# Kernel optimization log

Hardware: AMD Instinct MI355X
Metric: run time of the kernel (lower is better)

Reference implementation:

```python
import jax, jax.numpy as jnp
import numpy as np

N = 50000      # nodes
E = 800000     # edges (before self loops)
IN = 128       # input_dim
H1, C1 = 4, 64   # conv1 heads, per-head channels (concat -> 256)
H2, C2 = 1, 64   # conv2 heads, per-head channels (concat=False -> 64)
EPS_BN = 1e-5
NEG_SLOPE = 0.2


def setup_inputs() -> dict:
    key = jax.random.key(0)
    ks = jax.random.split(key, 20)
    s = 0.05
    d = {}
    d["x"] = jax.random.normal(ks[0], (N, IN), dtype=jnp.float32)
    d["edge_index"] = jax.random.randint(ks[1], (2, E), 0, N, dtype=jnp.int32)
    # GATConv 1: lin weight [IN, H1*C1], att vectors [H1, C1], bias [H1*C1]
    d["W1"] = jax.random.normal(ks[2], (IN, H1 * C1), dtype=jnp.float32) * s
    d["a1_src"] = jax.random.normal(ks[3], (H1, C1), dtype=jnp.float32) * s
    d["a1_dst"] = jax.random.normal(ks[4], (H1, C1), dtype=jnp.float32) * s
    d["b1"] = jnp.zeros((H1 * C1,), jnp.float32)
    # GATConv 2 (concat=False): lin weight [H1*C1, H2*C2]
    d["W2"] = jax.random.normal(ks[5], (H1 * C1, H2 * C2), dtype=jnp.float32) * s
    d["a2_src"] = jax.random.normal(ks[6], (H2, C2), dtype=jnp.float32) * s
    d["a2_dst"] = jax.random.normal(ks[7], (H2, C2), dtype=jnp.float32) * s
    d["b2"] = jnp.zeros((C2,), jnp.float32)
    # projection Linear(output_dim -> input_dim)
    d["Wp"] = jax.random.normal(ks[8], (C2, IN), dtype=jnp.float32) * s
    d["bp"] = jnp.zeros((IN,), jnp.float32)
    # BatchNorm affine params
    d["g1"] = jnp.ones((H1 * C1,), jnp.float32); d["be1"] = jnp.zeros((H1 * C1,), jnp.float32)
    d["g2"] = jnp.ones((C2,), jnp.float32);      d["be2"] = jnp.zeros((C2,), jnp.float32)
    d["g3"] = jnp.ones((IN,), jnp.float32);      d["be3"] = jnp.zeros((IN,), jnp.float32)
    return d


def batch_norm(x, gamma, beta):
    mu = jnp.mean(x, axis=0, keepdims=True)
    var = jnp.var(x, axis=0, keepdims=True)
    return (x - mu) * jax.lax.rsqrt(var + EPS_BN) * gamma + beta


def gat_conv(x, src, dst, W, a_src, a_dst, bias, heads, out_ch, concat):
    n = x.shape[0]
    h = (x @ W).reshape(n, heads, out_ch)            # [N,H,C]
    alpha_s = jnp.einsum('nhc,hc->nh', h, a_src)     # [N,H]
    alpha_d = jnp.einsum('nhc,hc->nh', h, a_dst)
    e = jax.nn.leaky_relu(alpha_s[src] + alpha_d[dst], NEG_SLOPE)  # [E',H]
    # segment softmax over edges sharing the same destination node
    m = jax.ops.segment_max(e, dst, num_segments=n)
    m = jnp.where(jnp.isfinite(m), m, 0.0)
    ex = jnp.exp(e - m[dst])
    den = jax.ops.segment_sum(ex, dst, num_segments=n)
    alpha = ex / (den[dst] + 1e-16)                  # [E',H]
    msg = alpha[:, :, None] * h[src]                 # [E',H,C]
    out = jax.ops.segment_sum(msg, dst, num_segments=n)  # [N,H,C]
    if concat:
        out = out.reshape(n, heads * out_ch)
    else:
        out = out.mean(axis=1)
    return out + bias


def reference(x, edge_index, W1, a1_src, a1_dst, b1, W2, a2_src, a2_dst, b2,
              Wp, bp, g1, be1, g2, be2, g3, be3):
    n = x.shape[0]
    # PyG GATConv default add_self_loops=True
    loops = jnp.arange(n, dtype=edge_index.dtype)
    src = jnp.concatenate([edge_index[0], loops])
    dst = jnp.concatenate([edge_index[1], loops])
    h = gat_conv(x, src, dst, W1, a1_src, a1_dst, b1, H1, C1, True)
    h = jax.nn.elu(batch_norm(h, g1, be1))
    # dropout is a no-op in eval mode
    h = gat_conv(h, src, dst, W2, a2_src, a2_dst, b2, H2, C2, False)
    h = jax.nn.elu(batch_norm(h, g2, be2))
    h = h @ Wp + bp
    return batch_norm(h, g3, be3)
```

## Files before the change

kernel.cpp:

```cpp
#include <hip/hip_runtime.h>
#include <cstdint>
#include <cstddef>

#define NEG_SLOPE 0.2f
#define EPS_BN 1e-5f

typedef __bf16 bf16x8 __attribute__((ext_vector_type(8)));
typedef float  f32x4  __attribute__((ext_vector_type(4)));
typedef unsigned short ushort_t;

static __device__ __forceinline__ float lrelu(float x){ return x > 0.f ? x : NEG_SLOPE * x; }
static __device__ __forceinline__ float elu(float x){ return x > 0.f ? x : __expf(x) - 1.f; }

static __device__ __forceinline__ float bf2f(ushort_t u){
  union { unsigned i; float f; } c; c.i = ((unsigned)u) << 16; return c.f;
}
static __device__ __forceinline__ ushort_t f2bf(float f){
  unsigned u = __float_as_uint(f);
  u += 0x7fffu + ((u >> 16) & 1u);
  return (ushort_t)(u >> 16);
}
static __device__ __forceinline__ void unpk(unsigned u, float& lo, float& hi){
  lo = __uint_as_float(u << 16);
  hi = __uint_as_float(u & 0xffff0000u);
}

union BF8 { bf16x8 v; ushort_t u[8]; };

static inline int ceil_div(int a, int b){ return (a + b - 1) / b; }


static __device__ void packW_body(const float* W, ushort_t* Wp, int K, int Nn, int idx){
  int lane = idx & 63;
  int rest = idx >> 6;
  int KS = K >> 5;
  int s = rest % KS, t = rest / KS;
  int n  = t * 16 + (lane & 15);
  int k0 = s * 32 + (lane >> 4) * 8;
  ushort_t tmp[8];
  #pragma unroll
  for(int j = 0; j < 8; j++) tmp[j] = f2bf(W[(size_t)(k0 + j) * Nn + n]);
  uint4 pk;
  pk.x = tmp[0] | ((unsigned)tmp[1] << 16);
  pk.y = tmp[2] | ((unsigned)tmp[3] << 16);
  pk.z = tmp[4] | ((unsigned)tmp[5] << 16);
  pk.w = tmp[6] | ((unsigned)tmp[7] << 16);
  *reinterpret_cast<uint4*>(Wp + (size_t)idx * 8) = pk;
}

__global__ void init_kernel(unsigned* __restrict__ zbase, int ztotal,
                            const float* __restrict__ W1, const float* __restrict__ W2,
                            const float* __restrict__ W3, ushort_t* __restrict__ W1p,
                            ushort_t* __restrict__ W2p, ushort_t* __restrict__ W3p){
  int b = blockIdx.x;
  if(b < 28){
    int idx = b * 256 + threadIdx.x;
    if(idx < 4096)       packW_body(W1, W1p, 128, 256, idx);
    else if(idx < 6144)  packW_body(W2, W2p, 256, 64,  idx - 4096);
    else if(idx < 7168)  packW_body(W3, W3p, 64,  128, idx - 6144);
  } else {
    int i = (b - 28) * 256 + threadIdx.x;
    if(i < ztotal) zbase[i] = 0u;
  }
}


template<int K, int NT, int AMODE, int H>
static __device__ __forceinline__ void gemm_body(int bx, const void* __restrict__ Asrc,
                                                 const ushort_t* __restrict__ Bp,
                                                 ushort_t* __restrict__ C, int M,
                                                 const float* __restrict__ scale,
                                                 const float* __restrict__ shift,
                                                 const float* __restrict__ a_src,
                                                 const float* __restrict__ a_dst,
                                                 float* __restrict__ as_,
                                                 float* __restrict__ ad_){
  constexpr int KS = K >> 5;
  int lane = threadIdx.x & 63, wv = threadIdx.x >> 6;
  int row0 = bx * 64 + wv * 16;
  int mi = lane & 15, q = lane >> 4;
  int arow = row0 + mi; if(arow > M - 1) arow = M - 1;
  const bf16x8* bbase = reinterpret_cast<const bf16x8*>(Bp) + lane;
  f32x4 acc[NT] = {};
  #pragma unroll
  for(int s = 0; s < KS; s++){
    BF8 cv;
    if(AMODE == 0){
      const float* ap = (const float*)Asrc + (size_t)arow * K + s * 32 + q * 8;
      float4 u0 = *reinterpret_cast<const float4*>(ap);
      float4 u1 = *reinterpret_cast<const float4*>(ap + 4);
      cv.u[0] = f2bf(u0.x); cv.u[1] = f2bf(u0.y); cv.u[2] = f2bf(u0.z); cv.u[3] = f2bf(u0.w);
      cv.u[4] = f2bf(u1.x); cv.u[5] = f2bf(u1.y); cv.u[6] = f2bf(u1.z); cv.u[7] = f2bf(u1.w);
    } else {
      const ushort_t* ap = (const ushort_t*)Asrc + (size_t)arow * K + s * 32 + q * 8;
      uint4 u = *reinterpret_cast<const uint4*>(ap);
      int c0 = s * 32 + q * 8;
      float4 sc0 = *reinterpret_cast<const float4*>(scale + c0);
      float4 sc1 = *reinterpret_cast<const float4*>(scale + c0 + 4);
      float4 sh0 = *reinterpret_cast<const float4*>(shift + c0);
      float4 sh1 = *reinterpret_cast<const float4*>(shift + c0 + 4);
      float a, b;
      unpk(u.x, a, b); cv.u[0] = f2bf(elu(a * sc0.x + sh0.x)); cv.u[1] = f2bf(elu(b * sc0.y + sh0.y));
      unpk(u.y, a, b); cv.u[2] = f2bf(elu(a * sc0.z + sh0.z)); cv.u[3] = f2bf(elu(b * sc0.w + sh0.w));
      unpk(u.z, a, b); cv.u[4] = f2bf(elu(a * sc1.x + sh1.x)); cv.u[5] = f2bf(elu(b * sc1.y + sh1.y));
      unpk(u.w, a, b); cv.u[6] = f2bf(elu(a * sc1.z + sh1.z)); cv.u[7] = f2bf(elu(b * sc1.w + sh1.w));
    }
    bf16x8 af = cv.v;
    #pragma unroll
    for(int t = 0; t < NT; t++){
      bf16x8 bfr = bbase[((size_t)t * KS + s) * 64];
      acc[t] = __builtin_amdgcn_mfma_f32_16x16x32_bf16(af, bfr, acc[t], 0, 0, 0);
    }
  }
  #pragma unroll
  for(int t = 0; t < NT; t++){
    #pragma unroll
    for(int r = 0; r < 4; r++){
      int gr = row0 + q * 4 + r;
      if(gr < M) C[(size_t)gr * (NT * 16) + t * 16 + mi] = f2bf(acc[t][r]);
    }
  }
  if(H > 0){
    #pragma unroll
    for(int hh = 0; hh < H; hh++){
      #pragma unroll
      for(int r = 0; r < 4; r++){
        float ps = 0.f, pd = 0.f;
        #pragma unroll
        for(int tt = 0; tt < 4; tt++){
          int t = hh * 4 + tt;
          float av = acc[t][r];
          int c = t * 16 + mi;
          ps += av * a_src[c];
          pd += av * a_dst[c];
        }
        #pragma unroll
        for(int off = 1; off < 16; off <<= 1){
          ps += __shfl_xor(ps, off);
          pd += __shfl_xor(pd, off);
        }
        int gr = row0 + q * 4 + r;
        if(mi == 0 && gr < M){
          as_[(size_t)gr * H + hh] = ps;
          ad_[(size_t)gr * H + hh] = pd;
        }
      }
    }
  }
}

template<int K, int NT, int AMODE, int H>
__global__ __launch_bounds__(256) void gemm_kernel(const void* __restrict__ Asrc,
                                                   const ushort_t* __restrict__ Bp,
                                                   ushort_t* __restrict__ C, int M,
                                                   const float* __restrict__ scale,
                                                   const float* __restrict__ shift,
                                                   const float* __restrict__ a_src,
                                                   const float* __restrict__ a_dst,
                                                   float* __restrict__ as_,
                                                   float* __restrict__ ad_){
  gemm_body<K, NT, AMODE, H>(blockIdx.x, Asrc, Bp, C, M, scale, shift, a_src, a_dst, as_, ad_);
}

__global__ __launch_bounds__(256) void hist_gemm1_kernel(int GB, const int* __restrict__ ei,
                                                         int* __restrict__ deg, int E, int N,
                                                         const float* __restrict__ x,
                                                         const ushort_t* __restrict__ W1p,
                                                         ushort_t* __restrict__ h1b,
                                                         const float* __restrict__ a1s,
                                                         const float* __restrict__ a1d,
                                                         float* __restrict__ as_,
                                                         float* __restrict__ ad_){
  int b = blockIdx.x;
  if(b < GB){
    gemm_body<128, 16, 0, 4>(b, x, W1p, h1b, N, nullptr, nullptr, a1s, a1d, as_, ad_);
  } else {
    int e = (b - GB) * 256 + threadIdx.x;
    if(e < E + N){
      int d = (e < E) ? ei[E + e] : (e - E);
      atomicAdd(&deg[d], 1);
    }
  }
}


__global__ __launch_bounds__(256) void scan1_kernel(const int* __restrict__ deg, int* __restrict__ rowptr,
                                                    int* __restrict__ partials,
                                                    unsigned* __restrict__ tick, int n){
  int t = threadIdx.x, lane = t & 63, wv = t >> 6;
  int base = blockIdx.x * 2048 + t * 8;
  int v[8]; int run = 0;
  #pragma unroll
  for(int k = 0; k < 8; k++){ int i = base + k; v[k] = (i < n) ? deg[i] : 0; run += v[k]; }
  int sc = run;
  #pragma unroll
  for(int off = 1; off < 64; off <<= 1){
    int u = __shfl_up(sc, off);
    if(lane >= off) sc += u;
  }
  __shared__ int wtot[4], woff[4];
  __shared__ bool slast;
  if(lane == 63) wtot[wv] = sc;
  __syncthreads();
  if(t == 0){
    int a = 0;
    #pragma unroll
    for(int i = 0; i < 4; i++){ woff[i] = a; a += wtot[i]; }
    partials[blockIdx.x] = a;
  }
  __syncthreads();
  int excl = (sc - run) + woff[wv];
  #pragma unroll
  for(int k = 0; k < 8; k++){
    int i = base + k;
    if(i < n){ rowptr[i] = excl; excl += v[k]; }
  }
  if(t == 0){
    __threadfence();
    slast = (atomicAdd(tick, 1u) == (unsigned)(gridDim.x - 1));
  }
  __syncthreads();
  if(slast && t < 64){
    int nb = gridDim.x;
    int pv = (t < nb) ? atomicAdd(&partials[t], 0) : 0;
    int psc = pv;
    #pragma unroll
    for(int off = 1; off < 64; off <<= 1){
      int u = __shfl_up(psc, off);
      if(t >= off) psc += u;
    }
    if(t < nb) partials[t] = psc - pv;
  }
}

__global__ void scatter_kernel(const int* __restrict__ ei, int* __restrict__ rowptr,
                               const int* __restrict__ part, int* __restrict__ col, int E, int N){
  int e = blockIdx.x * 256 + threadIdx.x;
  if(e >= E + N) return;
  int s, d;
  if(e < E){ s = ei[e]; d = ei[E + e]; } else { s = e - E; d = e - E; }
  int pos = atomicAdd(&rowptr[d], 1) + part[d >> 11];
  col[pos] = s;
}


__global__ __launch_bounds__(256) void gat_agg4_kernel(const ushort_t* __restrict__ hfeat,
                                                       const float* __restrict__ as_,
                                                       const float* __restrict__ ad_,
                                                       const int* __restrict__ rowptr,
                                                       const int* __restrict__ part,
                                                       const int* __restrict__ col,
                                                       const float* __restrict__ bias,
                                                       ushort_t* __restrict__ out, int N){
  int wid = threadIdx.x >> 6, lane = threadIdx.x & 63;
  int n = blockIdx.x * 4 + wid;
  if(n > N - 1) n = N - 1;
  int start = n ? rowptr[n - 1] + part[(n - 1) >> 11] : 0;
  int end   = rowptr[n] + part[n >> 11];
  int g = lane >> 5, l = lane & 31, hidx = l >> 3;
  float adh = ad_[(size_t)n * 4 + hidx];
  float den = 0.f;
  float acc[8] = {};
  int last = end - 1;
  auto body = [&](int j){
    bool live = j < end;
    int jc = live ? j : last;
    int s = col[jc];
    float w = live ? __expf(lrelu(as_[(size_t)s * 4 + hidx] + adh)) : 0.f;
    uint4 u = *reinterpret_cast<const uint4*>(hfeat + (size_t)s * 256 + 8 * l);
    den += w;
    float a, b;
    unpk(u.x, a, b); acc[0] += w * a; acc[1] += w * b;
    unpk(u.y, a, b); acc[2] += w * a; acc[3] += w * b;
    unpk(u.z, a, b); acc[4] += w * a; acc[5] += w * b;
    unpk(u.w, a, b); acc[6] += w * a; acc[7] += w * b;
  };
  for(int j = start + g; j < end; j += 8){
    body(j); body(j + 2); body(j + 4); body(j + 6);
  }
  den += __shfl_xor(den, 32);
  #pragma unroll
  for(int k = 0; k < 8; k++) acc[k] += __shfl_xor(acc[k], 32);
  float dinv = 1.f / (den + 1e-16f);
  int cbase = 8 * l + g * 4;
  ushort_t o0 = f2bf(acc[g * 4 + 0] * dinv + bias[cbase + 0]);
  ushort_t o1 = f2bf(acc[g * 4 + 1] * dinv + bias[cbase + 1]);
  ushort_t o2 = f2bf(acc[g * 4 + 2] * dinv + bias[cbase + 2]);
  ushort_t o3 = f2bf(acc[g * 4 + 3] * dinv + bias[cbase + 3]);
  uint2 pk; pk.x = o0 | ((unsigned)o1 << 16); pk.y = o2 | ((unsigned)o3 << 16);
  *reinterpret_cast<uint2*>(out + (size_t)n * 256 + cbase) = pk;
}


__global__ __launch_bounds__(256) void gat_agg1_kernel(const ushort_t* __restrict__ hfeat,
                                                       const float* __restrict__ as_,
                                                       const float* __restrict__ ad_,
                                                       const int* __restrict__ rowptr,
                                                       const int* __restrict__ part,
                                                       const int* __restrict__ col,
                                                       const float* __restrict__ bias,
                                                       ushort_t* __restrict__ out, int N){
  int wid = threadIdx.x >> 6, lane = threadIdx.x & 63;
  int n = blockIdx.x * 4 + wid;
  if(n > N - 1) n = N - 1;
  int start = n ? rowptr[n - 1] + part[(n - 1) >> 11] : 0;
  int end   = rowptr[n] + part[n >> 11];
  int g = lane >> 4, l = lane & 15;
  float adn = ad_[n];
  float den = 0.f;
  float acc[4] = {};
  int last = end - 1;
  auto body = [&](int j){
    bool live = j < end;
    int jc = live ? j : last;
    int s = col[jc];
    float w = live ? __expf(lrelu(as_[s] + adn)) : 0.f;
    uint2 u = *reinterpret_cast<const uint2*>(hfeat + (size_t)s * 64 + 4 * l);
    den += w;
    float a, b;
    unpk(u.x, a, b); acc[0] += w * a; acc[1] += w * b;
    unpk(u.y, a, b); acc[2] += w * a; acc[3] += w * b;
  };
  for(int j = start + g; j < end; j += 16){
    body(j); body(j + 4); body(j + 8); body(j + 12);
  }
  den += __shfl_xor(den, 16); den += __shfl_xor(den, 32);
  #pragma unroll
  for(int k = 0; k < 4; k++){
    acc[k] += __shfl_xor(acc[k], 16);
    acc[k] += __shfl_xor(acc[k], 32);
  }
  float dinv = 1.f / (den + 1e-16f);
  if(g == 0){
    ushort_t o0 = f2bf(acc[0] * dinv + bias[4 * l + 0]);
    ushort_t o1 = f2bf(acc[1] * dinv + bias[4 * l + 1]);
    ushort_t o2 = f2bf(acc[2] * dinv + bias[4 * l + 2]);
    ushort_t o3 = f2bf(acc[3] * dinv + bias[4 * l + 3]);
    uint2 pk; pk.x = o0 | ((unsigned)o1 << 16); pk.y = o2 | ((unsigned)o3 << 16);
    *reinterpret_cast<uint2*>(out + (size_t)n * 64 + 4 * l) = pk;
  }
}


template<int C>
__global__ __launch_bounds__(256) void colstats_fin_kernel(const ushort_t* __restrict__ x, int N,
                                                           float* __restrict__ stats,
                                                           const float* __restrict__ gamma,
                                                           const float* __restrict__ beta,
                                                           float* __restrict__ scale,
                                                           float* __restrict__ shift,
                                                           unsigned* __restrict__ ticket, int nblk){
  constexpr int TPR = C / 8;
  constexpr int RPB = 256 / TPR;
  int t = threadIdx.x;
  int c0 = (t % TPR) * 8, rg = t / TPR;
  float sum[8] = {}, sq[8] = {};
  for(int r = blockIdx.x * RPB + rg; r < N; r += gridDim.x * RPB){
    uint4 u = *reinterpret_cast<const uint4*>(x + (size_t)r * C + c0);
    float a, b;
    unpk(u.x, a, b); sum[0] += a; sq[0] += a * a; sum[1] += b; sq[1] += b * b;
    unpk(u.y, a, b); sum[2] += a; sq[2] += a * a; sum[3] += b; sq[3] += b * b;
    unpk(u.z, a, b); sum[4] += a; sq[4] += a * a; sum[5] += b; sq[5] += b * b;
    unpk(u.w, a, b); sum[6] += a; sq[6] += a * a; sum[7] += b; sq[7] += b * b;
  }
  __shared__ float red[2][256][8];
  #pragma unroll
  for(int k = 0; k < 8; k++){ red[0][t][k] = sum[k]; red[1][t][k] = sq[k]; }
  __syncthreads();
  if(t < C){
    int tr = t >> 3, k = t & 7;
    float S = 0.f, Q = 0.f;
    for(int g2 = 0; g2 < RPB; g2++){
      S += red[0][g2 * TPR + tr][k];
      Q += red[1][g2 * TPR + tr][k];
    }
    atomicAdd(&stats[t], S);
    atomicAdd(&stats[C + t], Q);
  }
  __shared__ bool is_last;
  __syncthreads();
  if(t == 0){
    __threadfence();
    is_last = (atomicAdd(ticket, 1u) == (unsigned)(nblk - 1));
  }
  __syncthreads();
  if(is_last && t < C){
    float S = atomicAdd(&stats[t], 0.f);
    float Q = atomicAdd(&stats[C + t], 0.f);
    float invN = 1.f / (float)N;
    float mu = S * invN;
    float var = Q * invN - mu * mu;
    float rs = rsqrtf(var + EPS_BN);
    float scl = rs * gamma[t];
    scale[t] = scl;
    shift[t] = beta[t] - mu * scl;
  }
}


__global__ void bn3_kernel(const ushort_t* __restrict__ x, const float* __restrict__ scale,
                           const float* __restrict__ shift, float* __restrict__ y, long total4){
  long i = (long)blockIdx.x * 256 + threadIdx.x;
  if(i >= total4) return;
  long e0 = i * 4;
  int c0 = (int)(e0 & 127);
  uint2 u = *reinterpret_cast<const uint2*>(x + e0);
  float4 sc = *reinterpret_cast<const float4*>(scale + c0);
  float4 sh = *reinterpret_cast<const float4*>(shift + c0);
  float a, b;
  float4 o;
  unpk(u.x, a, b); o.x = a * sc.x + sh.x; o.y = b * sc.y + sh.y;
  unpk(u.y, a, b); o.z = a * sc.z + sh.z; o.w = b * sc.w + sh.w;
  *reinterpret_cast<float4*>(y + e0) = o;
}


extern "C" void kernel_launch(void* const* d_in, const int* in_sizes, int n_in,
                              void* d_out, int out_size, void* d_ws, size_t ws_size,
                              hipStream_t stream){
  const float* x   = (const float*)d_in[0];
  const int*   ei  = (const int*)  d_in[1];
  const float* W1  = (const float*)d_in[2];
  const float* a1s = (const float*)d_in[3];
  const float* a1d = (const float*)d_in[4];
  const float* b1  = (const float*)d_in[5];
  const float* W2  = (const float*)d_in[6];
  const float* a2s = (const float*)d_in[7];
  const float* a2d = (const float*)d_in[8];
  const float* b2  = (const float*)d_in[9];
  const float* Wp  = (const float*)d_in[10];
  const float* g1  = (const float*)d_in[12]; const float* be1 = (const float*)d_in[13];
  const float* g2  = (const float*)d_in[14]; const float* be2 = (const float*)d_in[15];
  const float* g3  = (const float*)d_in[16]; const float* be3 = (const float*)d_in[17];
  float* out = (float*)d_out;

  const int N  = in_sizes[0] / 128;
  const int E  = in_sizes[1] / 2;
  const int EP = E + N;
  const int Mpad = ((N + 63) / 64) * 64;
  const int NB = ceil_div(N, 2048);
  const int GB = Mpad / 64;
  const int HB = ceil_div(EP, 256);

  char* p = (char*)d_ws;
  auto carve = [&](size_t bytes) -> char* {
    char* r = p; p += (bytes + 255) & ~(size_t)255; return r;
  };
  float* meta   = (float*)carve(2048 * 4);
  int*   deg    = (int*)carve((size_t)N * 4);
  int*   rowptr = (int*)carve((size_t)(N + 1) * 4);
  int*   col    = (int*)carve((size_t)EP * 4);
  int*   part   = (int*)carve(64 * 4);
  float* as_    = (float*)carve((size_t)N * 4 * 4);
  float* ad_    = (float*)carve((size_t)N * 4 * 4);
  ushort_t* W1p = (ushort_t*)carve((size_t)128 * 256 * 2);
  ushort_t* W2p = (ushort_t*)carve((size_t)256 * 64 * 2);
  ushort_t* W3p = (ushort_t*)carve((size_t)64 * 128 * 2);
  ushort_t* h1b   = (ushort_t*)carve((size_t)Mpad * 256 * 2);
  ushort_t* out1b = (ushort_t*)carve((size_t)Mpad * 256 * 2);
  ushort_t* h2b   = (ushort_t*)carve((size_t)Mpad * 64 * 2);
  ushort_t* out2b = (ushort_t*)carve((size_t)Mpad * 64 * 2);
  ushort_t* h3b   = (ushort_t*)carve((size_t)Mpad * 128 * 2);

  float* stats1 = meta;        float* scale1 = meta + 512;  float* shift1 = meta + 768;
  float* stats2 = meta + 1024; float* scale2 = meta + 1152; float* shift2 = meta + 1216;
  float* stats3 = meta + 1280; float* scale3 = meta + 1536; float* shift3 = meta + 1664;
  unsigned* tick = (unsigned*)(meta + 1792);

  init_kernel<<<28 + ceil_div(N + 2048, 256), 256, 0, stream>>>((unsigned*)meta, N + 2048,
                                                                W1, W2, Wp, W1p, W2p, W3p);
  hist_gemm1_kernel<<<GB + HB, 256, 0, stream>>>(GB, ei, deg, E, N, x, W1p, h1b, a1s, a1d, as_, ad_);
  scan1_kernel<<<NB, 256, 0, stream>>>(deg, rowptr, part, tick + 3, N);
  scatter_kernel<<<HB, 256, 0, stream>>>(ei, rowptr, part, col, E, N);
  gat_agg4_kernel<<<ceil_div(N, 4), 256, 0, stream>>>(h1b, as_, ad_, rowptr, part, col, b1, out1b, N);
  colstats_fin_kernel<256><<<512, 256, 0, stream>>>(out1b, N, stats1, g1, be1, scale1, shift1, tick + 0, 512);
  gemm_kernel<256, 4, 1, 1><<<GB, 256, 0, stream>>>(out1b, W2p, h2b, N, scale1, shift1, a2s, a2d, as_, ad_);
  gat_agg1_kernel<<<ceil_div(N, 4), 256, 0, stream>>>(h2b, as_, ad_, rowptr, part, col, b2, out2b, N);
  colstats_fin_kernel<64><<<512, 256, 0, stream>>>(out2b, N, stats2, g2, be2, scale2, shift2, tick + 1, 512);
  gemm_kernel<64, 8, 1, 0><<<GB, 256, 0, stream>>>(out2b, W3p, h3b, N, scale2, shift2, nullptr, nullptr, nullptr, nullptr);
  colstats_fin_kernel<128><<<512, 256, 0, stream>>>(h3b, N, stats3, g3, be3, scale3, shift3, tick + 2, 512);
  bn3_kernel<<<ceil_div(N * 128 / 4, 256), 256, 0, stream>>>(h3b, scale3, shift3, out, (long)N * 32);
}
```

Baseline: 418.3 us.

## Fuse BatchNorm column statistics into aggregation and GEMM epilogues

```diff
diff --git a/kernel.cpp b/kernel.cpp
--- a/kernel.cpp
+++ b/kernel.cpp
@@ -7,14 +7,12 @@
 
 typedef __bf16 bf16x8 __attribute__((ext_vector_type(8)));
 typedef float  f32x4  __attribute__((ext_vector_type(4)));
+typedef float  f32x2  __attribute__((ext_vector_type(2)));
 typedef unsigned short ushort_t;
 
 static __device__ __forceinline__ float lrelu(float x){ return x > 0.f ? x : NEG_SLOPE * x; }
 static __device__ __forceinline__ float elu(float x){ return x > 0.f ? x : __expf(x) - 1.f; }
 
-static __device__ __forceinline__ float bf2f(ushort_t u){
-  union { unsigned i; float f; } c; c.i = ((unsigned)u) << 16; return c.f;
-}
 static __device__ __forceinline__ ushort_t f2bf(float f){
   unsigned u = __float_as_uint(f);
   u += 0x7fffu + ((u >> 16) & 1u);
@@ -23,6 +21,12 @@
 static __device__ __forceinline__ void unpk(unsigned u, float& lo, float& hi){
   lo = __uint_as_float(u << 16);
   hi = __uint_as_float(u & 0xffff0000u);
+}
+static __device__ __forceinline__ f32x2 unpk2(unsigned u){
+  f32x2 r;
+  r.x = __uint_as_float(u << 16);
+  r.y = __uint_as_float(u & 0xffff0000u);
+  return r;
 }
 
 union BF8 { bf16x8 v; ushort_t u[8]; };
@@ -65,7 +69,7 @@
 }
 
 
-template<int K, int NT, int AMODE, int H>
+template<int K, int NT, int AMODE, int H, int STATS>
 static __device__ __forceinline__ void gemm_body(int bx, const void* __restrict__ Asrc,
                                                  const ushort_t* __restrict__ Bp,
                                                  ushort_t* __restrict__ C, int M,
@@ -74,7 +78,14 @@
                                                  const float* __restrict__ a_src,
                                                  const float* __restrict__ a_dst,
                                                  float* __restrict__ as_,
-                                                 float* __restrict__ ad_){
+                                                 float* __restrict__ ad_,
+                                                 float* __restrict__ rep,
+                                                 const float* __restrict__ gamma,
+                                                 const float* __restrict__ beta,
+                                                 float* __restrict__ scaleO,
+                                                 float* __restrict__ shiftO,
+                                                 unsigned* __restrict__ tick,
+                                                 int nblk){
   constexpr int KS = K >> 5;
   int lane = threadIdx.x & 63, wv = threadIdx.x >> 6;
   int row0 = bx * 64 + wv * 16;
@@ -147,9 +158,56 @@
       }
     }
   }
-}
-
-template<int K, int NT, int AMODE, int H>
+  if(STATS){
+    constexpr int CC = NT * 16;
+    __shared__ float lsum[4][CC], lsq[4][CC];
+    #pragma unroll
+    for(int t = 0; t < NT; t++){
+      float s_ = 0.f, q_ = 0.f;
+      #pragma unroll
+      for(int r = 0; r < 4; r++){
+        int gr = row0 + q * 4 + r;
+        float v = (gr < M) ? acc[t][r] : 0.f;
+        s_ += v; q_ += v * v;
+      }
+      s_ += __shfl_xor(s_, 16); s_ += __shfl_xor(s_, 32);
+      q_ += __shfl_xor(q_, 16); q_ += __shfl_xor(q_, 32);
+      if(lane < 16){ lsum[wv][t * 16 + lane] = s_; lsq[wv][t * 16 + lane] = q_; }
+    }
+    __syncthreads();
+    int t = threadIdx.x;
+    if(t < CC){
+      float S = lsum[0][t] + lsum[1][t] + lsum[2][t] + lsum[3][t];
+      float Q = lsq[0][t] + lsq[1][t] + lsq[2][t] + lsq[3][t];
+      int ri = (bx & 31) * (2 * CC);
+      atomicAdd(&rep[ri + t], S);
+      atomicAdd(&rep[ri + CC + t], Q);
+    }
+    __shared__ bool lastb;
+    __syncthreads();
+    if(t == 0){
+      __threadfence();
+      lastb = (atomicAdd(tick, 1u) == (unsigned)(nblk - 1));
+    }
+    __syncthreads();
+    if(lastb && t < CC){
+      float S = 0.f, Q = 0.f;
+      for(int r2 = 0; r2 < 32; r2++){
+        S += atomicAdd(&rep[r2 * (2 * CC) + t], 0.f);
+        Q += atomicAdd(&rep[r2 * (2 * CC) + CC + t], 0.f);
+      }
+      float invN = 1.f / (float)M;
+      float mu = S * invN;
+      float var = Q * invN - mu * mu;
+      float rs = rsqrtf(var + EPS_BN);
+      float scl = rs * gamma[t];
+      scaleO[t] = scl;
+      shiftO[t] = beta[t] - mu * scl;
+    }
+  }
+}
+
+template<int K, int NT, int AMODE, int H, int STATS>
 __global__ __launch_bounds__(256) void gemm_kernel(const void* __restrict__ Asrc,
                                                    const ushort_t* __restrict__ Bp,
                                                    ushort_t* __restrict__ C, int M,
@@ -158,8 +216,15 @@
                                                    const float* __restrict__ a_src,
                                                    const float* __restrict__ a_dst,
                                                    float* __restrict__ as_,
-                                                   float* __restrict__ ad_){
-  gemm_body<K, NT, AMODE, H>(blockIdx.x, Asrc, Bp, C, M, scale, shift, a_src, a_dst, as_, ad_);
+                                                   float* __restrict__ ad_,
+                                                   float* __restrict__ rep,
+                                                   const float* __restrict__ gamma,
+                                                   const float* __restrict__ beta,
+                                                   float* __restrict__ scaleO,
+                                                   float* __restrict__ shiftO,
+                                                   unsigned* __restrict__ tick){
+  gemm_body<K, NT, AMODE, H, STATS>(blockIdx.x, Asrc, Bp, C, M, scale, shift, a_src, a_dst,
+                                    as_, ad_, rep, gamma, beta, scaleO, shiftO, tick, gridDim.x);
 }
 
 __global__ __launch_bounds__(256) void hist_gemm1_kernel(int GB, const int* __restrict__ ei,
@@ -173,7 +238,8 @@
                                                          float* __restrict__ ad_){
   int b = blockIdx.x;
   if(b < GB){
-    gemm_body<128, 16, 0, 4>(b, x, W1p, h1b, N, nullptr, nullptr, a1s, a1d, as_, ad_);
+    gemm_body<128, 16, 0, 4, 0>(b, x, W1p, h1b, N, nullptr, nullptr, a1s, a1d, as_, ad_,
+                                nullptr, nullptr, nullptr, nullptr, nullptr, nullptr, 0);
   } else {
     int e = (b - GB) * 256 + threadIdx.x;
     if(e < E + N){
@@ -251,44 +317,92 @@
                                                        const int* __restrict__ part,
                                                        const int* __restrict__ col,
                                                        const float* __restrict__ bias,
-                                                       ushort_t* __restrict__ out, int N){
+                                                       ushort_t* __restrict__ out, int N,
+                                                       float* __restrict__ rep,
+                                                       const float* __restrict__ gamma,
+                                                       const float* __restrict__ beta,
+                                                       float* __restrict__ scaleO,
+                                                       float* __restrict__ shiftO,
+                                                       unsigned* __restrict__ tick){
   int wid = threadIdx.x >> 6, lane = threadIdx.x & 63;
-  int n = blockIdx.x * 4 + wid;
-  if(n > N - 1) n = N - 1;
+  int n0 = blockIdx.x * 4 + wid;
+  bool orig = n0 < N;
+  int n = orig ? n0 : N - 1;
   int start = n ? rowptr[n - 1] + part[(n - 1) >> 11] : 0;
   int end   = rowptr[n] + part[n >> 11];
   int g = lane >> 5, l = lane & 31, hidx = l >> 3;
   float adh = ad_[(size_t)n * 4 + hidx];
   float den = 0.f;
-  float acc[8] = {};
-  int last = end - 1;
+  f32x2 acc2[4] = {};
   auto body = [&](int j){
-    bool live = j < end;
-    int jc = live ? j : last;
-    int s = col[jc];
-    float w = live ? __expf(lrelu(as_[(size_t)s * 4 + hidx] + adh)) : 0.f;
+    int s = col[j];
+    float w = __expf(lrelu(as_[(size_t)s * 4 + hidx] + adh));
     uint4 u = *reinterpret_cast<const uint4*>(hfeat + (size_t)s * 256 + 8 * l);
     den += w;
-    float a, b;
-    unpk(u.x, a, b); acc[0] += w * a; acc[1] += w * b;
-    unpk(u.y, a, b); acc[2] += w * a; acc[3] += w * b;
-    unpk(u.z, a, b); acc[4] += w * a; acc[5] += w * b;
-    unpk(u.w, a, b); acc[6] += w * a; acc[7] += w * b;
+    acc2[0] += unpk2(u.x) * w;
+    acc2[1] += unpk2(u.y) * w;
+    acc2[2] += unpk2(u.z) * w;
+    acc2[3] += unpk2(u.w) * w;
   };
-  for(int j = start + g; j < end; j += 8){
-    body(j); body(j + 2); body(j + 4); body(j + 6);
-  }
+  int j = start + g;
+  for(; j + 6 < end; j += 8){ body(j); body(j + 2); body(j + 4); body(j + 6); }
+  for(; j < end; j += 2) body(j);
   den += __shfl_xor(den, 32);
   #pragma unroll
-  for(int k = 0; k < 8; k++) acc[k] += __shfl_xor(acc[k], 32);
+  for(int k = 0; k < 4; k++){
+    acc2[k].x += __shfl_xor(acc2[k].x, 32);
+    acc2[k].y += __shfl_xor(acc2[k].y, 32);
+  }
   float dinv = 1.f / (den + 1e-16f);
   int cbase = 8 * l + g * 4;
-  ushort_t o0 = f2bf(acc[g * 4 + 0] * dinv + bias[cbase + 0]);
-  ushort_t o1 = f2bf(acc[g * 4 + 1] * dinv + bias[cbase + 1]);
-  ushort_t o2 = f2bf(acc[g * 4 + 2] * dinv + bias[cbase + 2]);
-  ushort_t o3 = f2bf(acc[g * 4 + 3] * dinv + bias[cbase + 3]);
-  uint2 pk; pk.x = o0 | ((unsigned)o1 << 16); pk.y = o2 | ((unsigned)o3 << 16);
-  *reinterpret_cast<uint2*>(out + (size_t)n * 256 + cbase) = pk;
+  f32x2 p0 = g ? acc2[2] : acc2[0];
+  f32x2 p1 = g ? acc2[3] : acc2[1];
+  float o0 = p0.x * dinv + bias[cbase + 0];
+  float o1 = p0.y * dinv + bias[cbase + 1];
+  float o2 = p1.x * dinv + bias[cbase + 2];
+  float o3 = p1.y * dinv + bias[cbase + 3];
+  if(orig){
+    uint2 pk;
+    pk.x = f2bf(o0) | ((unsigned)f2bf(o1) << 16);
+    pk.y = f2bf(o2) | ((unsigned)f2bf(o3) << 16);
+    *reinterpret_cast<uint2*>(out + (size_t)n * 256 + cbase) = pk;
+  }
+  __shared__ float lsum[4][256], lsq[4][256];
+  float z0 = orig ? o0 : 0.f, z1 = orig ? o1 : 0.f, z2 = orig ? o2 : 0.f, z3 = orig ? o3 : 0.f;
+  lsum[wid][cbase + 0] = z0; lsq[wid][cbase + 0] = z0 * z0;
+  lsum[wid][cbase + 1] = z1; lsq[wid][cbase + 1] = z1 * z1;
+  lsum[wid][cbase + 2] = z2; lsq[wid][cbase + 2] = z2 * z2;
+  lsum[wid][cbase + 3] = z3; lsq[wid][cbase + 3] = z3 * z3;
+  __syncthreads();
+  int t = threadIdx.x;
+  {
+    float S = lsum[0][t] + lsum[1][t] + lsum[2][t] + lsum[3][t];
+    float Q = lsq[0][t] + lsq[1][t] + lsq[2][t] + lsq[3][t];
+    int ri = ((int)blockIdx.x & 31) * 512;
+    atomicAdd(&rep[ri + t], S);
+    atomicAdd(&rep[ri + 256 + t], Q);
+  }
+  __shared__ bool lastb;
+  __syncthreads();
+  if(t == 0){
+    __threadfence();
+    lastb = (atomicAdd(tick, 1u) == (unsigned)(gridDim.x - 1));
+  }
+  __syncthreads();
+  if(lastb){
+    float S = 0.f, Q = 0.f;
+    for(int r2 = 0; r2 < 32; r2++){
+      S += atomicAdd(&rep[r2 * 512 + t], 0.f);
+      Q += atomicAdd(&rep[r2 * 512 + 256 + t], 0.f);
+    }
+    float invN = 1.f / (float)N;
+    float mu = S * invN;
+    float var = Q * invN - mu * mu;
+    float rs = rsqrtf(var + EPS_BN);
+    float scl = rs * gamma[t];
+    scaleO[t] = scl;
+    shiftO[t] = beta[t] - mu * scl;
+  }
 }
 
 
@@ -299,119 +413,111 @@
                                                        const int* __restrict__ part,
                                                        const int* __restrict__ col,
                                                        const float* __restrict__ bias,
-                                                       ushort_t* __restrict__ out, int N){
+                                                       ushort_t* __restrict__ out, int N,
+                                                       float* __restrict__ rep,
+                                                       const float* __restrict__ gamma,
+                                                       const float* __restrict__ beta,
+                                                       float* __restrict__ scaleO,
+                                                       float* __restrict__ shiftO,
+                                                       unsigned* __restrict__ tick){
   int wid = threadIdx.x >> 6, lane = threadIdx.x & 63;
-  int n = blockIdx.x * 4 + wid;
-  if(n > N - 1) n = N - 1;
+  int n0 = blockIdx.x * 4 + wid;
+  bool orig = n0 < N;
+  int n = orig ? n0 : N - 1;
   int start = n ? rowptr[n - 1] + part[(n - 1) >> 11] : 0;
   int end   = rowptr[n] + part[n >> 11];
   int g = lane >> 4, l = lane & 15;
   float adn = ad_[n];
   float den = 0.f;
-  float acc[4] = {};
-  int last = end - 1;
+  f32x2 acc2[2] = {};
   auto body = [&](int j){
-    bool live = j < end;
-    int jc = live ? j : last;
-    int s = col[jc];
-    float w = live ? __expf(lrelu(as_[s] + adn)) : 0.f;
+    int s = col[j];
+    float w = __expf(lrelu(as_[s] + adn));
     uint2 u = *reinterpret_cast<const uint2*>(hfeat + (size_t)s * 64 + 4 * l);
     den += w;
-    float a, b;
-    unpk(u.x, a, b); acc[0] += w * a; acc[1] += w * b;
-    unpk(u.y, a, b); acc[2] += w * a; acc[3] += w * b;
+    acc2[0] += unpk2(u.x) * w;
+    acc2[1] += unpk2(u.y) * w;
   };
-  for(int j = start + g; j < end; j += 16){
-    body(j); body(j + 4); body(j + 8); body(j + 12);
-  }
+  int j = start + g;
+  for(; j + 4 < end; j += 8){ body(j); body(j + 4); }
+  if(j < end) body(j);
   den += __shfl_xor(den, 16); den += __shfl_xor(den, 32);
   #pragma unroll
-  for(int k = 0; k < 4; k++){
-    acc[k] += __shfl_xor(acc[k], 16);
-    acc[k] += __shfl_xor(acc[k], 32);
+  for(int k = 0; k < 2; k++){
+    acc2[k].x += __shfl_xor(acc2[k].x, 16); acc2[k].x += __shfl_xor(acc2[k].x, 32);
+    acc2[k].y += __shfl_xor(acc2[k].y, 16); acc2[k].y += __shfl_xor(acc2[k].y, 32);
   }
   float dinv = 1.f / (den + 1e-16f);
+  float o0 = acc2[0].x * dinv + bias[4 * l + 0];
+  float o1 = acc2[0].y * dinv + bias[4 * l + 1];
+  float o2 = acc2[1].x * dinv + bias[4 * l + 2];
+  float o3 = acc2[1].y * dinv + bias[4 * l + 3];
+  if(g == 0 && orig){
+    uint2 pk;
+    pk.x = f2bf(o0) | ((unsigned)f2bf(o1) << 16);
+    pk.y = f2bf(o2) | ((unsigned)f2bf(o3) << 16);
+    *reinterpret_cast<uint2*>(out + (size_t)n * 64 + 4 * l) = pk;
+  }
+  __shared__ float lsum[4][64], lsq[4][64];
   if(g == 0){
-    ushort_t o0 = f2bf(acc[0] * dinv + bias[4 * l + 0]);
-    ushort_t o1 = f2bf(acc[1] * dinv + bias[4 * l + 1]);
-    ushort_t o2 = f2bf(acc[2] * dinv + bias[4 * l + 2]);
-    ushort_t o3 = f2bf(acc[3] * dinv + bias[4 * l + 3]);
-    uint2 pk; pk.x = o0 | ((unsigned)o1 << 16); pk.y = o2 | ((unsigned)o3 << 16);
-    *reinterpret_cast<uint2*>(out + (size_t)n * 64 + 4 * l) = pk;
-  }
-}
-
-
-template<int C>
-__global__ __launch_bounds__(256) void colstats_fin_kernel(const ushort_t* __restrict__ x, int N,
-                                                           float* __restrict__ stats,
-                                                           const float* __restrict__ gamma,
-                                                           const float* __restrict__ beta,
-                                                           float* __restrict__ scale,
-                                                           float* __restrict__ shift,
-                                                           unsigned* __restrict__ ticket, int nblk){
-  constexpr int TPR = C / 8;
-  constexpr int RPB = 256 / TPR;
+    float z0 = orig ? o0 : 0.f, z1 = orig ? o1 : 0.f, z2 = orig ? o2 : 0.f, z3 = orig ? o3 : 0.f;
+    lsum[wid][4 * l + 0] = z0; lsq[wid][4 * l + 0] = z0 * z0;
+    lsum[wid][4 * l + 1] = z1; lsq[wid][4 * l + 1] = z1 * z1;
+    lsum[wid][4 * l + 2] = z2; lsq[wid][4 * l + 2] = z2 * z2;
+    lsum[wid][4 * l + 3] = z3; lsq[wid][4 * l + 3] = z3 * z3;
+  }
+  __syncthreads();
   int t = threadIdx.x;
-  int c0 = (t % TPR) * 8, rg = t / TPR;
-  float sum[8] = {}, sq[8] = {};
-  for(int r = blockIdx.x * RPB + rg; r < N; r += gridDim.x * RPB){
-    uint4 u = *reinterpret_cast<const uint4*>(x + (size_t)r * C + c0);
-    float a, b;
-    unpk(u.x, a, b); sum[0] += a; sq[0] += a * a; sum[1] += b; sq[1] += b * b;
-    unpk(u.y, a, b); sum[2] += a; sq[2] += a * a; sum[3] += b; sq[3] += b * b;
-    unpk(u.z, a, b); sum[4] += a; sq[4] += a * a; sum[5] += b; sq[5] += b * b;
-    unpk(u.w, a, b); sum[6] += a; sq[6] += a * a; sum[7] += b; sq[7] += b * b;
-  }
-  __shared__ float red[2][256][8];
-  #pragma unroll
-  for(int k = 0; k < 8; k++){ red[0][t][k] = sum[k]; red[1][t][k] = sq[k]; }
-  __syncthreads();
-  if(t < C){
-    int tr = t >> 3, k = t & 7;
-    float S = 0.f, Q = 0.f;
-    for(int g2 = 0; g2 < RPB; g2++){
-      S += red[0][g2 * TPR + tr][k];
-      Q += red[1][g2 * TPR + tr][k];
-    }
-    atomicAdd(&stats[t], S);
-    atomicAdd(&stats[C + t], Q);
-  }
-  __shared__ bool is_last;
+  if(t < 64){
+    float S = lsum[0][t] + lsum[1][t] + lsum[2][t] + lsum[3][t];
+    float Q = lsq[0][t] + lsq[1][t] + lsq[2][t] + lsq[3][t];
+    int ri = ((int)blockIdx.x & 31) * 128;
+    atomicAdd(&rep[ri + t], S);
+    atomicAdd(&rep[ri + 64 + t], Q);
+  }
+  __shared__ bool lastb;
   __syncthreads();
   if(t == 0){
     __threadfence();
-    is_last = (atomicAdd(ticket, 1u) == (unsigned)(nblk - 1));
-  }
-  __syncthreads();
-  if(is_last && t < C){
-    float S = atomicAdd(&stats[t], 0.f);
-    float Q = atomicAdd(&stats[C + t], 0.f);
+    lastb = (atomicAdd(tick, 1u) == (unsigned)(gridDim.x - 1));
+  }
+  __syncthreads();
+  if(lastb && t < 64){
+    float S = 0.f, Q = 0.f;
+    for(int r2 = 0; r2 < 32; r2++){
+      S += atomicAdd(&rep[r2 * 128 + t], 0.f);
+      Q += atomicAdd(&rep[r2 * 128 + 64 + t], 0.f);
+    }
     float invN = 1.f / (float)N;
     float mu = S * invN;
     float var = Q * invN - mu * mu;
     float rs = rsqrtf(var + EPS_BN);
     float scl = rs * gamma[t];
-    scale[t] = scl;
-    shift[t] = beta[t] - mu * scl;
+    scaleO[t] = scl;
+    shiftO[t] = beta[t] - mu * scl;
   }
 }
 
 
 __global__ void bn3_kernel(const ushort_t* __restrict__ x, const float* __restrict__ scale,
-                           const float* __restrict__ shift, float* __restrict__ y, long total4){
+                           const float* __restrict__ shift, float* __restrict__ y, long total8){
   long i = (long)blockIdx.x * 256 + threadIdx.x;
-  if(i >= total4) return;
-  long e0 = i * 4;
+  if(i >= total8) return;
+  long e0 = i * 8;
   int c0 = (int)(e0 & 127);
-  uint2 u = *reinterpret_cast<const uint2*>(x + e0);
-  float4 sc = *reinterpret_cast<const float4*>(scale + c0);
-  float4 sh = *reinterpret_cast<const float4*>(shift + c0);
+  uint4 u = *reinterpret_cast<const uint4*>(x + e0);
+  float4 sc0 = *reinterpret_cast<const float4*>(scale + c0);
+  float4 sc1 = *reinterpret_cast<const float4*>(scale + c0 + 4);
+  float4 sh0 = *reinterpret_cast<const float4*>(shift + c0);
+  float4 sh1 = *reinterpret_cast<const float4*>(shift + c0 + 4);
   float a, b;
-  float4 o;
-  unpk(u.x, a, b); o.x = a * sc.x + sh.x; o.y = b * sc.y + sh.y;
-  unpk(u.y, a, b); o.z = a * sc.z + sh.z; o.w = b * sc.w + sh.w;
-  *reinterpret_cast<float4*>(y + e0) = o;
+  float4 o0, o1;
+  unpk(u.x, a, b); o0.x = a * sc0.x + sh0.x; o0.y = b * sc0.y + sh0.y;
+  unpk(u.y, a, b); o0.z = a * sc0.z + sh0.z; o0.w = b * sc0.w + sh0.w;
+  unpk(u.z, a, b); o1.x = a * sc1.x + sh1.x; o1.y = b * sc1.y + sh1.y;
+  unpk(u.w, a, b); o1.z = a * sc1.z + sh1.z; o1.w = b * sc1.w + sh1.w;
+  *reinterpret_cast<float4*>(y + e0) = o0;
+  *reinterpret_cast<float4*>(y + e0 + 4) = o1;
 }
 
 
@@ -446,7 +552,7 @@
   auto carve = [&](size_t bytes) -> char* {
     char* r = p; p += (bytes + 255) & ~(size_t)255; return r;
   };
-  float* meta   = (float*)carve(2048 * 4);
+  float* meta   = (float*)carve(30720 * 4);
   int*   deg    = (int*)carve((size_t)N * 4);
   int*   rowptr = (int*)carve((size_t)(N + 1) * 4);
   int*   col    = (int*)carve((size_t)EP * 4);
@@ -462,22 +568,28 @@
   ushort_t* out2b = (ushort_t*)carve((size_t)Mpad * 64 * 2);
   ushort_t* h3b   = (ushort_t*)carve((size_t)Mpad * 128 * 2);
 
-  float* stats1 = meta;        float* scale1 = meta + 512;  float* shift1 = meta + 768;
-  float* stats2 = meta + 1024; float* scale2 = meta + 1152; float* shift2 = meta + 1216;
-  float* stats3 = meta + 1280; float* scale3 = meta + 1536; float* shift3 = meta + 1664;
-  unsigned* tick = (unsigned*)(meta + 1792);
-
-  init_kernel<<<28 + ceil_div(N + 2048, 256), 256, 0, stream>>>((unsigned*)meta, N + 2048,
-                                                                W1, W2, Wp, W1p, W2p, W3p);
+  float* rep1 = meta;
+  float* rep2 = meta + 16384;
+  float* rep3 = meta + 20480;
+  float* scale1 = meta + 28672; float* shift1 = meta + 28928;
+  float* scale2 = meta + 29184; float* shift2 = meta + 29248;
+  float* scale3 = meta + 29312; float* shift3 = meta + 29440;
+  unsigned* tick = (unsigned*)(meta + 29568);
+
+  init_kernel<<<28 + ceil_div(30720 + N, 256), 256, 0, stream>>>((unsigned*)meta, 30720 + N,
+                                                                 W1, W2, Wp, W1p, W2p, W3p);
   hist_gemm1_kernel<<<GB + HB, 256, 0, stream>>>(GB, ei, deg, E, N, x, W1p, h1b, a1s, a1d, as_, ad_);
   scan1_kernel<<<NB, 256, 0, stream>>>(deg, rowptr, part, tick + 3, N);
   scatter_kernel<<<HB, 256, 0, stream>>>(ei, rowptr, part, col, E, N);
-  gat_agg4_kernel<<<ceil_div(N, 4), 256, 0, stream>>>(h1b, as_, ad_, rowptr, part, col, b1, out1b, N);
-  colstats_fin_kernel<256><<<512, 256, 0, stream>>>(out1b, N, stats1, g1, be1, scale1, shift1, tick + 0, 512);
-  gemm_kernel<256, 4, 1, 1><<<GB, 256, 0, stream>>>(out1b, W2p, h2b, N, scale1, shift1, a2s, a2d, as_, ad_);
-  gat_agg1_kernel<<<ceil_div(N, 4), 256, 0, stream>>>(h2b, as_, ad_, rowptr, part, col, b2, out2b, N);
-  colstats_fin_kernel<64><<<512, 256, 0, stream>>>(out2b, N, stats2, g2, be2, scale2, shift2, tick + 1, 512);
-  gemm_kernel<64, 8, 1, 0><<<GB, 256, 0, stream>>>(out2b, W3p, h3b, N, scale2, shift2, nullptr, nullptr, nullptr, nullptr);
-  colstats_fin_kernel<128><<<512, 256, 0, stream>>>(h3b, N, stats3, g3, be3, scale3, shift3, tick + 2, 512);
-  bn3_kernel<<<ceil_div(N * 128 / 4, 256), 256, 0, stream>>>(h3b, scale3, shift3, out, (long)N * 32);
-}
+  gat_agg4_kernel<<<ceil_div(N, 4), 256, 0, stream>>>(h1b, as_, ad_, rowptr, part, col, b1, out1b, N,
+                                                      rep1, g1, be1, scale1, shift1, tick + 0);
+  gemm_kernel<256, 4, 1, 1, 0><<<GB, 256, 0, stream>>>(out1b, W2p, h2b, N, scale1, shift1,
+                                                       a2s, a2d, as_, ad_,
+                                                       nullptr, nullptr, nullptr, nullptr, nullptr, nullptr);
+  gat_agg1_kernel<<<ceil_div(N, 4), 256, 0, stream>>>(h2b, as_, ad_, rowptr, part, col, b2, out2b, N,
+                                                      rep2, g2, be2, scale2, shift2, tick + 1);
+  gemm_kernel<64, 8, 1, 0, 1><<<GB, 256, 0, stream>>>(out2b, W3p, h3b, N, scale2, shift2,
+                                                      nullptr, nullptr, nullptr, nullptr,
+                                                      rep3, g3, be3, scale3, shift3, tick + 2);
+  bn3_kernel<<<ceil_div(N * 16, 256), 256, 0, stream>>>(h3b, scale3, shift3, out, (long)N * 16);
+}
```

Measured after the change: 1.075 ms. 2.57x slower.
